# Optimization experiments

Hardware: AMD Instinct MI355X
Metric: run time of the kernel (lower is better)

Reference implementation:

```python
import jax, jax.numpy as jnp
import numpy as np

EMBED_DIM = 1280
NUM_STATES = 20
B, L = 8, 1024

# upper-triangular (offset=1) indices, matching torch.triu_indices(N, N, offset=1)
_IU, _JU = np.triu_indices(NUM_STATES, k=1)


def setup_inputs() -> dict:
    key = jax.random.key(0)
    ks = jax.random.split(key, 4)
    d = EMBED_DIM
    n = NUM_STATES
    m = n * (n - 1) // 2
    s = 1.0 / np.sqrt(d)
    return {
        "hx": jax.random.normal(ks[0], (B, L, d), dtype=jnp.float32),
        "dense_w": jax.random.normal(ks[1], (d, d), dtype=jnp.float32) * s,
        "dense_b": jnp.zeros((d,), dtype=jnp.float32),
        "ln_w": jnp.ones((d,), dtype=jnp.float32),
        "ln_b": jnp.zeros((d,), dtype=jnp.float32),
        "theta_w": jax.random.normal(ks[2], (d, n), dtype=jnp.float32) * s,
        "theta_b": jnp.zeros((n,), dtype=jnp.float32),
        "Theta_w": jax.random.normal(ks[3], (d, m), dtype=jnp.float32) * s,
        "Theta_b": jnp.zeros((m,), dtype=jnp.float32),
    }


def _layer_norm(x, w, b, eps=1e-5):
    mu = jnp.mean(x, axis=-1, keepdims=True)
    var = jnp.mean(jnp.square(x - mu), axis=-1, keepdims=True)
    return (x - mu) * jax.lax.rsqrt(var + eps) * w + b


def reference(hx, dense_w, dense_b, ln_w, ln_b, theta_w, theta_b, Theta_w, Theta_b):
    n = NUM_STATES
    # dense -> exact gelu (ESM uses erf gelu) -> layer norm
    h = hx @ dense_w + dense_b                        # [B,L,D]
    h = _layer_norm(jax.nn.gelu(h, approximate=False), ln_w, ln_b)
    pi = jax.nn.softmax(h @ theta_w + theta_b, axis=-1)          # [B,L,N]
    Theta = jax.nn.softplus(h @ Theta_w + Theta_b)               # [B,L,N*(N-1)/2]
    # scatter upper triangle, then symmetrize
    S = jnp.zeros((*h.shape[:2], n, n), dtype=h.dtype).at[..., _IU, _JU].set(Theta)
    S = S + jnp.swapaxes(S, -2, -1)                              # [B,L,N,N]
    # diag(1/sqrt(pi)) @ S @ diag(sqrt(pi)) == elementwise row/col scaling
    pi_sqrt = jnp.sqrt(pi)
    Q = S * (pi_sqrt[..., None, :] / pi_sqrt[..., :, None])
    # Q - diag_embed(Q.sum(-1))
    Q = Q - Q.sum(axis=-1)[..., :, None] * jnp.eye(n, dtype=Q.dtype)
    return Q
```

## Files before the change

### kernel.cpp

```cpp
#include <hip/hip_runtime.h>
#include <hip/hip_bf16.h>
#include <math.h>

#define D 1280
#define NST 20
#define MTRI 190
#define NTOK 8192
#define NC 256

typedef __attribute__((ext_vector_type(4))) float f32x4;
typedef __attribute__((ext_vector_type(8))) __bf16 bf16x8;
typedef __attribute__((ext_vector_type(8))) unsigned short ushort8;
typedef __attribute__((ext_vector_type(4))) unsigned short bfu4;

__device__ __forceinline__ void gload_lds16(const void* g, void* l) {
    __builtin_amdgcn_global_load_lds(
        (const __attribute__((address_space(1))) void*)g,
        (__attribute__((address_space(3))) void*)l, 16, 0, 0);
}

__device__ __forceinline__ unsigned short f2bf(float x) {
    __hip_bfloat16 b = __float2bfloat16(x);
    return __builtin_bit_cast(unsigned short, b);
}
__device__ __forceinline__ float bf2f(unsigned short u) {
    unsigned int x = ((unsigned int)u) << 16;
    return __builtin_bit_cast(float, x);
}

__global__ __launch_bounds__(256) void tobf_kernel(
    const float* __restrict__ X, unsigned short* __restrict__ Y)
{
    const size_t i = ((size_t)blockIdx.x * 256 + threadIdx.x) * 8;
    float4 a = *(const float4*)(X + i);
    float4 b = *(const float4*)(X + i + 4);
    ushort8 u;
    u[0] = f2bf(a.x); u[1] = f2bf(a.y); u[2] = f2bf(a.z); u[3] = f2bf(a.w);
    u[4] = f2bf(b.x); u[5] = f2bf(b.y); u[6] = f2bf(b.z); u[7] = f2bf(b.w);
    *(ushort8*)(Y + i) = u;
}

__global__ __launch_bounds__(256) void transpose_w_kernel(
    const float* __restrict__ W, unsigned short* __restrict__ Wt)
{
    __shared__ float t[64][65];
    const int tid = threadIdx.x;
    const int k0 = blockIdx.x * 64, n0 = blockIdx.y * 64;
#pragma unroll
    for (int i = 0; i < 16; ++i) {
        int lin = i * 256 + tid;
        int r = lin >> 6, c = lin & 63;
        t[r][c] = W[(size_t)(k0 + r) * D + n0 + c];
    }
    __syncthreads();
#pragma unroll
    for (int i = 0; i < 16; ++i) {
        int lin = i * 256 + tid;
        int r = lin >> 6, c = lin & 63;
        Wt[(size_t)(n0 + r) * D + (k0 + c)] = f2bf(t[c][r]);
    }
}

__global__ __launch_bounds__(256) void build_wcat_kernel(
    const float* __restrict__ theta_w, const float* __restrict__ Theta_w,
    const float* __restrict__ ln_w,
    unsigned short* __restrict__ Wcat)
{
    const int col = threadIdx.x;
    const int k0  = blockIdx.x * 64;
    for (int kk = 0; kk < 64; kk += 8) {
        ushort8 u;
#pragma unroll
        for (int j = 0; j < 8; ++j) {
            int k = k0 + kk + j;
            float v = 0.0f;
            if (col < NST)             v = theta_w[(size_t)k * NST + col];
            else if (col < NST + MTRI) v = Theta_w[(size_t)k * MTRI + (col - NST)];
            u[j] = f2bf(ln_w[k] * v);
        }
        *(ushort8*)&Wcat[(size_t)col * D + k0 + kk] = u;
    }
}

__global__ __launch_bounds__(64) void build_uv_kernel(
    const unsigned short* __restrict__ Wcat,
    const float* __restrict__ theta_w, const float* __restrict__ Theta_w,
    const float* __restrict__ ln_b,
    const float* __restrict__ theta_b, const float* __restrict__ Theta_b,
    float* __restrict__ U, float* __restrict__ Vp)
{
    const int col  = blockIdx.x;
    const int lane = threadIdx.x;
    float u = 0.f, v = 0.f;
    for (int k = lane; k < D; k += 64) {
        u += bf2f(Wcat[(size_t)col * D + k]);
        float w = 0.f;
        if (col < NST)             w = theta_w[(size_t)k * NST + col];
        else if (col < NST + MTRI) w = Theta_w[(size_t)k * MTRI + (col - NST)];
        v += ln_b[k] * w;
    }
#pragma unroll
    for (int off = 1; off < 64; off <<= 1) {
        u += __shfl_xor(u, off);
        v += __shfl_xor(v, off);
    }
    if (lane == 0) {
        float b = 0.f;
        if (col < NST)             b = theta_b[col];
        else if (col < NST + MTRI) b = Theta_b[col - NST];
        U[col]  = u;
        Vp[col] = v + b;
    }
}

#define BKA 32

__global__ __launch_bounds__(512) void gemm_gelu_mfma_kernel(
    const unsigned short* __restrict__ Ab,
    const unsigned short* __restrict__ Wt,
    const float* __restrict__ bias,
    unsigned short* __restrict__ H)
{
    __shared__ unsigned short As[2][128 * BKA];
    __shared__ unsigned short Bs[2][64 * BKA];

    const int tid  = threadIdx.x;
    const int lane = tid & 63;
    const int w    = tid >> 6;
    const int wr   = w >> 1;
    const int wc   = w & 1;

    const int bid = blockIdx.x;
    const int swz = (bid & 7) * 160 + (bid >> 3);
    const int row0 = (swz / 20) * 128;
    const int col0 = (swz % 20) * 64;

    f32x4 acc[2][2];
#pragma unroll
    for (int m = 0; m < 2; ++m)
#pragma unroll
        for (int n = 0; n < 2; ++n) acc[m][n] = (f32x4)0.0f;

    const int sR = lane >> 2;
    const int sK = (lane & 3) * 8;
    const unsigned short* aSrc = &Ab[(size_t)(row0 + w * 16 + sR) * D + sK];
    const unsigned short* bSrc = &Wt[(size_t)(col0 + (w & 3) * 16 + sR) * D + sK];

    auto STAGE = [&](int b, int k0) {
        gload_lds16(aSrc + k0, &As[b][(w * 16) * BKA]);
        if (w < 4) gload_lds16(bSrc + k0, &Bs[b][(w * 16) * BKA]);
    };

    STAGE(0, 0);
    __syncthreads();

    const int fr = lane & 15;
    const int fk = (lane >> 4) * 8;

    for (int t = 0; t < 40; ++t) {
        const int cur = t & 1;
        if (t < 39) STAGE(cur ^ 1, (t + 1) * BKA);

        bf16x8 af[2], bfv[2];
#pragma unroll
        for (int m = 0; m < 2; ++m)
            af[m] = *(const bf16x8*)&As[cur][(wr * 32 + m * 16 + fr) * BKA + fk];
#pragma unroll
        for (int n = 0; n < 2; ++n)
            bfv[n] = *(const bf16x8*)&Bs[cur][(wc * 32 + n * 16 + fr) * BKA + fk];
#pragma unroll
        for (int m = 0; m < 2; ++m)
#pragma unroll
            for (int n = 0; n < 2; ++n)
                acc[m][n] = __builtin_amdgcn_mfma_f32_16x16x32_bf16(
                    af[m], bfv[n], acc[m][n], 0, 0, 0);
        __syncthreads();
    }

    const int crow = (lane >> 4) * 4;
#pragma unroll
    for (int n = 0; n < 2; ++n) {
        const int col = col0 + wc * 32 + n * 16 + fr;
        const float bv = bias[col];
#pragma unroll
        for (int m = 0; m < 2; ++m) {
            const int rbase = row0 + wr * 32 + m * 16 + crow;
#pragma unroll
            for (int r = 0; r < 4; ++r) {
                float h = acc[m][n][r] + bv;
                float g = 0.5f * h * (1.0f + erff(h * 0.70710678118654752f));
                H[(size_t)(rbase + r) * D + col] = f2bf(g);
            }
        }
    }
}

__global__ __launch_bounds__(256) void ln_stats_kernel(
    const unsigned short* __restrict__ Hb, float2* __restrict__ stats)
{
    const int wave = threadIdx.x >> 6, lane = threadIdx.x & 63;
    const int row = blockIdx.x * 4 + wave;
    const unsigned short* src = Hb + (size_t)row * D;
    float sum = 0.f, sq = 0.f;
#pragma unroll
    for (int i = 0; i < 5; ++i) {
        bfu4 u = *(const bfu4*)(src + (size_t)(i * 64 + lane) * 4);
#pragma unroll
        for (int j = 0; j < 4; ++j) {
            float f = bf2f(u[j]);
            sum += f; sq += f * f;
        }
    }
#pragma unroll
    for (int off = 1; off < 64; off <<= 1) {
        sum += __shfl_xor(sum, off);
        sq  += __shfl_xor(sq, off);
    }
    if (lane == 0) {
        float mean = sum * (1.0f / D);
        float var  = sq * (1.0f / D) - mean * mean;
        stats[row] = make_float2(mean, rsqrtf(var + 1e-5f));
    }
}

__global__ __launch_bounds__(256) void head_mfma_kernel(
    const unsigned short* __restrict__ Hb,
    const float2* __restrict__ stats,
    const float* __restrict__ U, const float* __restrict__ Vp,
    const unsigned short* __restrict__ Wcat,
    float* __restrict__ Out)
{
    __shared__ unsigned short Bs[2][NC * 32];
    __shared__ unsigned short As[2][16 * 32];
    __shared__ float U_s[NC], V_s[NC];
    __shared__ float mean_s[16], inv_s[16];
    float (*th_l)[NST]  = (float (*)[NST])&Bs[0][0];
    float (*sp_l)[MTRI] = (float (*)[MTRI])((char*)&Bs[0][0] + 16 * NST * 4);
    float (*s_l)[NST]   = (float (*)[NST])((char*)&Bs[0][0] + 16 * NST * 4 + 16 * MTRI * 4);

    const int tid  = threadIdx.x;
    const int lane = tid & 63;
    const int wave = tid >> 6;
    const int bid  = blockIdx.x;
    const int swz  = (bid & 7) * 64 + (bid >> 3);
    const int g0   = swz * 16;

    U_s[tid] = U[tid];
    V_s[tid] = Vp[tid];
    if (tid < 16) {
        float2 s = stats[g0 + tid];
        mean_s[tid] = s.x;
        inv_s[tid]  = s.y;
    }

    auto STAGEB = [&](int b, int k0) {
#pragma unroll
        for (int i = 0; i < 4; ++i) {
            const int c0 = wave * 64 + i * 16;
            gload_lds16(&Wcat[(size_t)(c0 + (lane >> 2)) * D + k0 + (lane & 3) * 8],
                        &Bs[b][c0 * 32]);
        }
    };
    auto STAGEA = [&](int b, int k0) {
        if (wave == 0) {
            gload_lds16(&Hb[(size_t)(g0 + (lane >> 2)) * D + k0 + (lane & 3) * 8],
                        &As[b][0]);
        }
    };

    STAGEB(0, 0);
    STAGEA(0, 0);
    __syncthreads();

    f32x4 acc[4];
#pragma unroll
    for (int n = 0; n < 4; ++n) acc[n] = (f32x4)0.0f;

    const int fr = lane & 15;
    const int fk = (lane >> 4) * 8;

    for (int t = 0; t < 40; ++t) {
        const int cur = t & 1;
        if (t < 39) {
            STAGEB(cur ^ 1, (t + 1) * 32);
            STAGEA(cur ^ 1, (t + 1) * 32);
        }
        bf16x8 af = *(const bf16x8*)&As[cur][fr * 32 + fk];
#pragma unroll
        for (int n = 0; n < 4; ++n) {
            bf16x8 bfv = *(const bf16x8*)&Bs[cur][(wave * 64 + n * 16 + fr) * 32 + fk];
            acc[n] = __builtin_amdgcn_mfma_f32_16x16x32_bf16(af, bfv, acc[n], 0, 0, 0);
        }
        __syncthreads();
    }

    const int crow = (lane >> 4) * 4;
#pragma unroll
    for (int n = 0; n < 4; ++n) {
        const int col = wave * 64 + n * 16 + fr;
        const float Uc = U_s[col];
        const float Vc = V_s[col];
#pragma unroll
        for (int r = 0; r < 4; ++r) {
            const int row = crow + r;
            float v = inv_s[row] * (acc[n][r] - mean_s[row] * Uc) + Vc;
            if (col < NST) {
                th_l[row][col] = v;
            } else if (col < NST + MTRI) {
                sp_l[row][col - NST] = (v > 20.0f) ? v : log1pf(expf(v));
            }
        }
    }
    __syncthreads();

#pragma unroll
    for (int p = 0; p < 2; ++p) {
        const int r = p * 8 + wave * 2 + (lane >> 5);
        const int l = lane & 31;
        float v = (l < NST) ? th_l[r][l] : -1e30f;
        float m = v;
#pragma unroll
        for (int off = 16; off >= 1; off >>= 1) m = fmaxf(m, __shfl_xor(m, off));
        float e = (l < NST) ? __expf(v - m) : 0.0f;
        float s = e;
#pragma unroll
        for (int off = 16; off >= 1; off >>= 1) s += __shfl_xor(s, off);
        if (l < NST) s_l[r][l] = sqrtf(e / s);
    }
    __syncthreads();

#pragma unroll
    for (int base = 0; base < 320; base += 256) {
        const int idx = base + tid;
        if (idx < 320) {
            const int r = idx / NST;
            const int i = idx % NST;
            const float inv_si = 1.0f / s_l[r][i];
            float q[NST];
            float rowsum = 0.f;
#pragma unroll
            for (int j = 0; j < NST; ++j) {
                if (j == i) { q[j] = 0.f; continue; }
                int a = (i < j) ? i : j;
                int b = (i < j) ? j : i;
                int tix = a * NST - a * (a + 1) / 2 + (b - a - 1);
                float v = sp_l[r][tix] * s_l[r][j] * inv_si;
                q[j] = v;
                rowsum += v;
            }
            q[i] = -rowsum;
            float* dst = Out + (size_t)(g0 + r) * (NST * NST) + i * NST;
#pragma unroll
            for (int j4 = 0; j4 < 5; ++j4) {
                *(float4*)(dst + j4 * 4) =
                    make_float4(q[j4 * 4], q[j4 * 4 + 1], q[j4 * 4 + 2], q[j4 * 4 + 3]);
            }
        }
    }
}

extern "C" void kernel_launch(void* const* d_in, const int* in_sizes, int n_in,
                              void* d_out, int out_size, void* d_ws, size_t ws_size,
                              hipStream_t stream) {
    const float* hx      = (const float*)d_in[0];
    const float* dense_w = (const float*)d_in[1];
    const float* dense_b = (const float*)d_in[2];
    const float* ln_w    = (const float*)d_in[3];
    const float* ln_b    = (const float*)d_in[4];
    const float* theta_w = (const float*)d_in[5];
    const float* theta_b = (const float*)d_in[6];
    const float* Theta_w = (const float*)d_in[7];
    const float* Theta_b = (const float*)d_in[8];
    float* out = (float*)d_out;

    unsigned short* hxb  = (unsigned short*)d_ws;
    unsigned short* H    = hxb + (size_t)NTOK * D;
    unsigned short* Wt   = H + (size_t)NTOK * D;
    unsigned short* Wcat = Wt + (size_t)D * D;
    float2* stats        = (float2*)(Wcat + (size_t)NC * D);
    float* U             = (float*)(stats + NTOK);
    float* Vp            = U + NC;

    tobf_kernel<<<(NTOK * D) / 2048, 256, 0, stream>>>(hx, hxb);

    dim3 gridT(D / 64, D / 64);
    transpose_w_kernel<<<gridT, 256, 0, stream>>>(dense_w, Wt);
    build_wcat_kernel<<<D / 64, 256, 0, stream>>>(theta_w, Theta_w, ln_w, Wcat);
    build_uv_kernel<<<NC, 64, 0, stream>>>(Wcat, theta_w, Theta_w, ln_b,
                                           theta_b, Theta_b, U, Vp);

    gemm_gelu_mfma_kernel<<<1280, 512, 0, stream>>>(hxb, Wt, dense_b, H);

    ln_stats_kernel<<<NTOK / 4, 256, 0, stream>>>(H, stats);

    head_mfma_kernel<<<512, 256, 0, stream>>>(H, stats, U, Vp, Wcat, out);
}
```

Before: 135.0 us.

## Fuse bf16 input conversion and LayerNorm statistics into the dense GEMM

```diff
diff --git a/kernel.cpp b/kernel.cpp
--- a/kernel.cpp
+++ b/kernel.cpp
@@ -7,11 +7,11 @@
 #define MTRI 190
 #define NTOK 8192
 #define NC 256
+#define NCH 40
 
 typedef __attribute__((ext_vector_type(4))) float f32x4;
 typedef __attribute__((ext_vector_type(8))) __bf16 bf16x8;
 typedef __attribute__((ext_vector_type(8))) unsigned short ushort8;
-typedef __attribute__((ext_vector_type(4))) unsigned short bfu4;
 
 __device__ __forceinline__ void gload_lds16(const void* g, void* l) {
     __builtin_amdgcn_global_load_lds(
@@ -26,18 +26,6 @@
 __device__ __forceinline__ float bf2f(unsigned short u) {
     unsigned int x = ((unsigned int)u) << 16;
     return __builtin_bit_cast(float, x);
-}
-
-__global__ __launch_bounds__(256) void tobf_kernel(
-    const float* __restrict__ X, unsigned short* __restrict__ Y)
-{
-    const size_t i = ((size_t)blockIdx.x * 256 + threadIdx.x) * 8;
-    float4 a = *(const float4*)(X + i);
-    float4 b = *(const float4*)(X + i + 4);
-    ushort8 u;
-    u[0] = f2bf(a.x); u[1] = f2bf(a.y); u[2] = f2bf(a.z); u[3] = f2bf(a.w);
-    u[4] = f2bf(b.x); u[5] = f2bf(b.y); u[6] = f2bf(b.z); u[7] = f2bf(b.w);
-    *(ushort8*)(Y + i) = u;
 }
 
 __global__ __launch_bounds__(256) void transpose_w_kernel(
@@ -116,10 +104,11 @@
 #define BKA 32
 
 __global__ __launch_bounds__(512) void gemm_gelu_mfma_kernel(
-    const unsigned short* __restrict__ Ab,
+    const float* __restrict__ A,
     const unsigned short* __restrict__ Wt,
     const float* __restrict__ bias,
-    unsigned short* __restrict__ H)
+    unsigned short* __restrict__ H,
+    float* __restrict__ ps, float* __restrict__ pq)
 {
     __shared__ unsigned short As[2][128 * BKA];
     __shared__ unsigned short Bs[2][64 * BKA];
@@ -141,17 +130,30 @@
 #pragma unroll
         for (int n = 0; n < 2; ++n) acc[m][n] = (f32x4)0.0f;
 
+    const int aRow = tid >> 2;
+    const int aK8  = (tid & 3) * 8;
+    const float* aSrc = &A[(size_t)(row0 + aRow) * D + aK8];
+
     const int sR = lane >> 2;
     const int sK = (lane & 3) * 8;
-    const unsigned short* aSrc = &Ab[(size_t)(row0 + w * 16 + sR) * D + sK];
     const unsigned short* bSrc = &Wt[(size_t)(col0 + (w & 3) * 16 + sR) * D + sK];
 
-    auto STAGE = [&](int b, int k0) {
-        gload_lds16(aSrc + k0, &As[b][(w * 16) * BKA]);
-        if (w < 4) gload_lds16(bSrc + k0, &Bs[b][(w * 16) * BKA]);
+    auto STAGE_B = [&](int b, int k0) {
+        if (w < 4) gload_lds16(bSrc + k0, &Bs[b][((w & 3) * 16) * BKA]);
     };
-
-    STAGE(0, 0);
+    auto WRITE_A = [&](int b, const float4& f0, const float4& f1) {
+        ushort8 o;
+        o[0] = f2bf(f0.x); o[1] = f2bf(f0.y); o[2] = f2bf(f0.z); o[3] = f2bf(f0.w);
+        o[4] = f2bf(f1.x); o[5] = f2bf(f1.y); o[6] = f2bf(f1.z); o[7] = f2bf(f1.w);
+        *(ushort8*)&As[b][aRow * BKA + aK8] = o;
+    };
+
+    {
+        STAGE_B(0, 0);
+        float4 f0 = *(const float4*)(aSrc + 0);
+        float4 f1 = *(const float4*)(aSrc + 4);
+        WRITE_A(0, f0, f1);
+    }
     __syncthreads();
 
     const int fr = lane & 15;
@@ -159,7 +161,13 @@
 
     for (int t = 0; t < 40; ++t) {
         const int cur = t & 1;
-        if (t < 39) STAGE(cur ^ 1, (t + 1) * BKA);
+        float4 f0, f1;
+        if (t < 39) {
+            const int k0 = (t + 1) * BKA;
+            STAGE_B(cur ^ 1, k0);
+            f0 = *(const float4*)(aSrc + k0 + 0);
+            f1 = *(const float4*)(aSrc + k0 + 4);
+        }
 
         bf16x8 af[2], bfv[2];
 #pragma unroll
@@ -174,10 +182,18 @@
             for (int n = 0; n < 2; ++n)
                 acc[m][n] = __builtin_amdgcn_mfma_f32_16x16x32_bf16(
                     af[m], bfv[n], acc[m][n], 0, 0, 0);
+
+        if (t < 39) WRITE_A(cur ^ 1, f0, f1);
         __syncthreads();
     }
 
     const int crow = (lane >> 4) * 4;
+    float s_[2][4], q_[2][4];
+#pragma unroll
+    for (int m = 0; m < 2; ++m)
+#pragma unroll
+        for (int r = 0; r < 4; ++r) { s_[m][r] = 0.f; q_[m][r] = 0.f; }
+
 #pragma unroll
     for (int n = 0; n < 2; ++n) {
         const int col = col0 + wc * 32 + n * 16 + fr;
@@ -190,37 +206,49 @@
                 float h = acc[m][n][r] + bv;
                 float g = 0.5f * h * (1.0f + erff(h * 0.70710678118654752f));
                 H[(size_t)(rbase + r) * D + col] = f2bf(g);
-            }
-        }
-    }
-}
-
-__global__ __launch_bounds__(256) void ln_stats_kernel(
-    const unsigned short* __restrict__ Hb, float2* __restrict__ stats)
-{
-    const int wave = threadIdx.x >> 6, lane = threadIdx.x & 63;
-    const int row = blockIdx.x * 4 + wave;
-    const unsigned short* src = Hb + (size_t)row * D;
-    float sum = 0.f, sq = 0.f;
-#pragma unroll
-    for (int i = 0; i < 5; ++i) {
-        bfu4 u = *(const bfu4*)(src + (size_t)(i * 64 + lane) * 4);
-#pragma unroll
-        for (int j = 0; j < 4; ++j) {
-            float f = bf2f(u[j]);
-            sum += f; sq += f * f;
-        }
-    }
-#pragma unroll
-    for (int off = 1; off < 64; off <<= 1) {
-        sum += __shfl_xor(sum, off);
-        sq  += __shfl_xor(sq, off);
-    }
-    if (lane == 0) {
-        float mean = sum * (1.0f / D);
-        float var  = sq * (1.0f / D) - mean * mean;
-        stats[row] = make_float2(mean, rsqrtf(var + 1e-5f));
-    }
+                s_[m][r] += g;
+                q_[m][r] += g * g;
+            }
+        }
+    }
+#pragma unroll
+    for (int m = 0; m < 2; ++m)
+#pragma unroll
+        for (int r = 0; r < 4; ++r) {
+#pragma unroll
+            for (int off = 1; off < 16; off <<= 1) {
+                s_[m][r] += __shfl_xor(s_[m][r], off);
+                q_[m][r] += __shfl_xor(q_[m][r], off);
+            }
+        }
+    if (fr == 0) {
+        const int qd = lane >> 4;
+        const int ch = (swz % 20) * 2 + wc;
+#pragma unroll
+        for (int m = 0; m < 2; ++m)
+#pragma unroll
+            for (int r = 0; r < 4; ++r) {
+                const int row = row0 + wr * 32 + m * 16 + qd * 4 + r;
+                ps[(size_t)ch * NTOK + row] = s_[m][r];
+                pq[(size_t)ch * NTOK + row] = q_[m][r];
+            }
+    }
+}
+
+__global__ __launch_bounds__(256) void finalize_stats_kernel(
+    const float* __restrict__ ps, const float* __restrict__ pq,
+    float2* __restrict__ stats)
+{
+    const int row = blockIdx.x * 256 + threadIdx.x;
+    float s = 0.f, q = 0.f;
+#pragma unroll
+    for (int ch = 0; ch < NCH; ++ch) {
+        s += ps[(size_t)ch * NTOK + row];
+        q += pq[(size_t)ch * NTOK + row];
+    }
+    float mean = s * (1.0f / D);
+    float var  = q * (1.0f / D) - mean * mean;
+    stats[row] = make_float2(mean, rsqrtf(var + 1e-5f));
 }
 
 __global__ __launch_bounds__(256) void head_mfma_kernel(
@@ -373,15 +401,14 @@
     const float* Theta_b = (const float*)d_in[8];
     float* out = (float*)d_out;
 
-    unsigned short* hxb  = (unsigned short*)d_ws;
-    unsigned short* H    = hxb + (size_t)NTOK * D;
+    unsigned short* H    = (unsigned short*)d_ws;
     unsigned short* Wt   = H + (size_t)NTOK * D;
     unsigned short* Wcat = Wt + (size_t)D * D;
-    float2* stats        = (float2*)(Wcat + (size_t)NC * D);
+    float* ps            = (float*)(Wcat + (size_t)NC * D);
+    float* pq            = ps + (size_t)NCH * NTOK;
+    float2* stats        = (float2*)(pq + (size_t)NCH * NTOK);
     float* U             = (float*)(stats + NTOK);
     float* Vp            = U + NC;
-
-    tobf_kernel<<<(NTOK * D) / 2048, 256, 0, stream>>>(hx, hxb);
 
     dim3 gridT(D / 64, D / 64);
     transpose_w_kernel<<<gridT, 256, 0, stream>>>(dense_w, Wt);
@@ -389,9 +416,9 @@
     build_uv_kernel<<<NC, 64, 0, stream>>>(Wcat, theta_w, Theta_w, ln_b,
                                            theta_b, Theta_b, U, Vp);
 
-    gemm_gelu_mfma_kernel<<<1280, 512, 0, stream>>>(hxb, Wt, dense_b, H);
-
-    ln_stats_kernel<<<NTOK / 4, 256, 0, stream>>>(H, stats);
+    gemm_gelu_mfma_kernel<<<1280, 512, 0, stream>>>(hx, Wt, dense_b, H, ps, pq);
+
+    finalize_stats_kernel<<<NTOK / 256, 256, 0, stream>>>(ps, pq, stats);
 
     head_mfma_kernel<<<512, 256, 0, stream>>>(H, stats, U, Vp, Wcat, out);
 }
```

Result: slower. 151.7 us (+12.4%).
